# Performance work log

Hardware: AMD Instinct MI355X
Metric: run time of the kernel (lower is better)

## Reference

```python
import jax, jax.numpy as jnp
import numpy as np

B_GRAPHS, N2, FDIM, HEADS = 128, 32, 256, 4
TOTAL = 262144


def setup_inputs() -> dict:
    key = jax.random.key(0)
    ks = jax.random.split(key, 6)
    # sorted graph ids, guaranteed to cover all B_GRAPHS values
    batch = jnp.sort(jnp.concatenate([
        jax.random.randint(ks[0], (TOTAL - B_GRAPHS,), 0, B_GRAPHS),
        jnp.arange(B_GRAPHS)])).astype(jnp.int32)
    x = jax.random.normal(ks[1], (TOTAL, FDIM), jnp.float32)
    queries = jax.random.normal(ks[2], (1, N2, FDIM), jnp.float32)
    s = 1.0 / np.sqrt(FDIM)
    in_proj_w = jax.random.uniform(ks[3], (3 * FDIM, FDIM), jnp.float32, -s, s)
    in_proj_b = jnp.zeros((3 * FDIM,), jnp.float32)
    out_proj_w = jax.random.uniform(ks[4], (FDIM, FDIM), jnp.float32, -s, s)
    out_proj_b = jnp.zeros((FDIM,), jnp.float32)
    return {"x": x, "batch": batch, "queries": queries,
            "in_proj_w": in_proj_w, "in_proj_b": in_proj_b,
            "out_proj_w": out_proj_w, "out_proj_b": out_proj_b}


def reference(x, batch, queries, in_proj_w, in_proj_b, out_proj_w, out_proj_b):
    F = x.shape[-1]
    H = HEADS
    d = F // H
    B = int(batch.max()) + 1
    counts = jnp.bincount(batch, length=B)                      # [B]
    N_max = int(counts.max())
    offsets = jnp.concatenate([jnp.zeros((1,), counts.dtype), jnp.cumsum(counts)[:-1]])
    pos = jnp.arange(batch.shape[0]) - offsets[batch]           # position within segment
    # ragged -> padded scatter (equivalent of the python loop)
    x_padded = jnp.zeros((B, N_max, F), x.dtype).at[batch, pos].set(x)
    valid = jnp.arange(N_max)[None, :] < counts[:, None]        # [B, N_max], True = real token

    Wq, Wk, Wv = in_proj_w[:F], in_proj_w[F:2 * F], in_proj_w[2 * F:]
    bq, bk, bv = in_proj_b[:F], in_proj_b[F:2 * F], in_proj_b[2 * F:]

    scale = 1.0 / np.sqrt(d)
    q = (queries[0] @ Wq.T + bq).reshape(N2, H, d) * scale      # [N2, H, d] (shared over B)
    k = (x_padded @ Wk.T + bk).reshape(B, N_max, H, d)
    v = (x_padded @ Wv.T + bv).reshape(B, N_max, H, d)

    scores = jnp.einsum('qhd,bkhd->bhqk', q, k)                 # [B, H, N2, N_max]
    scores = jnp.where(valid[:, None, None, :], scores, -jnp.inf)
    attn = jax.nn.softmax(scores, axis=-1)
    out = jnp.einsum('bhqk,bkhd->bqhd', attn, v).reshape(B, N2, F)
    out = out @ out_proj_w.T + out_proj_b
    return out.reshape(B * N2, F)
```

## Files before the change

### kernel.cpp

```cpp
#include <hip/hip_runtime.h>
#include <hip/hip_bf16.h>

typedef __bf16 bf16x8 __attribute__((ext_vector_type(8)));
typedef float  f32x4  __attribute__((ext_vector_type(4)));

#define MFMA16(a,b,c) __builtin_amdgcn_mfma_f32_16x16x32_bf16((a),(b),(c),0,0,0)

__device__ __forceinline__ unsigned short f2bf(float f){
  unsigned int u = __float_as_uint(f);
  u += 0x7fffu + ((u >> 16) & 1u);
  return (unsigned short)(u >> 16);
}

__device__ __forceinline__ unsigned int cvtpk(float lo, float hi){
  unsigned int r;
  asm("v_cvt_pk_bf16_f32 %0, %1, %2" : "=v"(r) : "v"(lo), "v"(hi));
  return r;
}

__device__ __forceinline__ void block_sync(){
  asm volatile("s_waitcnt lgkmcnt(0)" ::: "memory");
  __builtin_amdgcn_s_barrier();
}

constexpr float SCALE_LOG2E = 0.125f * 1.4426950408889634f;

__global__ void k_prep(const float* __restrict__ queries, const float* __restrict__ ipw,
                       const float* __restrict__ ipb, const float* __restrict__ opw,
                       const float* __restrict__ opb, const int* __restrict__ batch,
                       int total, int* __restrict__ starts,
                       unsigned short* __restrict__ AqF,
                       unsigned short* __restrict__ Cmat, float* __restrict__ cvec)
{
  __shared__ __align__(16) float sh[256];
  __shared__ __align__(16) float sh2[256];
  const int t = threadIdx.x, bid = blockIdx.x;

  if (bid < 32){
    const int q = bid;
    sh[t] = queries[q*256 + t];
    __syncthreads();
    const float* wr = ipw + (size_t)t*256;
    float acc = 0.f;
    #pragma unroll 8
    for (int j = 0; j < 256; j += 4){
      float4 wv = *reinterpret_cast<const float4*>(wr + j);
      float4 qv = *reinterpret_cast<const float4*>(&sh[j]);
      acc += wv.x*qv.x + wv.y*qv.y + wv.z*qv.z + wv.w*qv.w;
    }
    sh2[t] = acc + ipb[t];
    __syncthreads();
    #pragma unroll
    for (int h = 0; h < 4; h++){
      const float* wk = ipw + (size_t)(256 + h*64)*256 + t;
      float a2 = 0.f;
      #pragma unroll 8
      for (int d = 0; d < 64; d++) a2 += sh2[h*64 + d] * wk[(size_t)d*256];
      const int dst = ((h*2 + (q>>4))*8 + (t>>5))*512 + (((t>>3)&3)*16 + (q&15))*8 + (t&7);
      AqF[dst] = f2bf(a2 * SCALE_LOG2E);
    }
  } else if (bid < 288){
    const int g = bid - 32;
    sh[t] = opw[(size_t)g*256 + t];
    __syncthreads();
    #pragma unroll
    for (int h = 0; h < 4; h++){
      const float* wv = ipw + (size_t)(512 + h*64)*256 + t;
      float acc = 0.f;
      #pragma unroll 8
      for (int d = 0; d < 64; d++) acc += wv[(size_t)d*256] * sh[h*64 + d];
      Cmat[(size_t)g*1024 + h*256 + t] = f2bf(acc);
    }
    sh2[t] = ipb[512 + t] * sh[t];
    __syncthreads();
    for (int off = 128; off > 0; off >>= 1){
      if (t < off) sh2[t] += sh2[t + off];
      __syncthreads();
    }
    if (t == 0) cvec[g] = sh2[0] + opb[g];
  } else {
    const int sb = bid - 288;
    const int i0 = sb*1024 + t*4;
    if (i0 + 3 < total){
      if (i0 == 0) starts[0] = 0;
      const int4 b4 = *reinterpret_cast<const int4*>(batch + i0);
      if (b4.y != b4.x) starts[b4.y] = i0 + 1;
      if (b4.z != b4.y) starts[b4.z] = i0 + 2;
      if (b4.w != b4.z) starts[b4.w] = i0 + 3;
      if (i0 + 4 < total){
        const int nxt = batch[i0 + 4];
        if (nxt != b4.w) starts[nxt] = i0 + 4;
      } else {
        starts[128] = total;
      }
    }
  }
}


#define LOADC(c_) { \
  const int c0_ = (c_)*32; \
  _Pragma("unroll") \
  for (int n = 0; n < 4; n++){ \
    int nl_ = c0_ + nq*4 + n; nl_ = nl_ < cnt-1 ? nl_ : cnt-1; \
    rA[n] = *reinterpret_cast<const float2*>(xg + (size_t)nl_*256 + fp*2); } }

#define STAGE(xsP, xtP) { \
  _Pragma("unroll") \
  for (int n = 0; n < 4; n++) \
    *reinterpret_cast<unsigned int*>(&(xsP)[(nq*4 + n)*264 + fp*2]) = cvtpk(rA[n].x, rA[n].y); \
  { const int f0_ = fp*2; \
    uint2 w0_; w0_.x = cvtpk(rA[0].x, rA[1].x); w0_.y = cvtpk(rA[2].x, rA[3].x); \
    *reinterpret_cast<uint2*>(reinterpret_cast<char*>(xtP) + ((f0_*80 + nq*8) ^ (((f0_>>2)&7)<<4))) = w0_; \
    const int f1_ = fp*2 + 1; \
    uint2 w1_; w1_.x = cvtpk(rA[0].y, rA[1].y); w1_.y = cvtpk(rA[2].y, rA[3].y); \
    *reinterpret_cast<uint2*>(reinterpret_cast<char*>(xtP) + ((f1_*80 + nq*8) ^ (((f1_>>2)&7)<<4))) = w1_; } }

__global__ __launch_bounds__(1024, 4) void k_attn(
    const float* __restrict__ x, const int* __restrict__ starts,
    const unsigned short* __restrict__ AqF,
    float* __restrict__ partO, float* __restrict__ partL)
{
  __shared__ __align__(16) unsigned short xsub[2][32*264];
  __shared__ __align__(16) unsigned short xT  [3][256*40];
  __shared__ __align__(16) unsigned short Plds[2][128*40];
  __shared__ __align__(16) float lred[2][128];

  const int tid = threadIdx.x;
  const int wave = tid >> 6, lane = tid & 63, lg = lane >> 4, li = lane & 15;
  const int rg = wave >> 1, bsel = wave & 1;
  const int fs = wave * 16;
  const int nq = tid >> 7, fp = tid & 127;
  const int bid = blockIdx.x;
  const int g = bid >> 1, s = bid & 1;
  const int s0 = starts[g], s1 = starts[g+1];
  const int cntg = s1 - s0;
  const int half = (cntg + 1) >> 1;
  const int nstart = s0 + s*half;
  int cnt = cntg - s*half; cnt = cnt < 0 ? 0 : (cnt > half ? half : cnt);
  const int chunks = (cnt + 31) >> 5;
  const float* xg = x + (size_t)nstart*256;

  bf16x8 bfragS[8];
  #pragma unroll
  for (int kb = 0; kb < 8; kb++)
    bfragS[kb] = *reinterpret_cast<const bf16x8*>(AqF + (size_t)(rg*8 + kb)*512 + lane*8);

  f32x4 oacc[8];
  #pragma unroll
  for (int i = 0; i < 8; i++) oacc[i] = f32x4{0.f,0.f,0.f,0.f};
  float rsum = 0.f;

  float2 rA[4];
  if (chunks > 0){
    LOADC(0);
    STAGE(xsub[0], xT[0]);
    if (chunks > 1) LOADC(1);
    block_sync();
  }

  int cur3 = 0;
  for (int c = 0; c < chunks; ++c){
    const int cur2 = c & 1;
    const int nxt3 = (cur3 == 2) ? 0 : cur3 + 1;

    f32x4 sacc = f32x4{0.f,0.f,0.f,0.f};
    __builtin_amdgcn_s_setprio(1);
    #pragma unroll
    for (int kb = 0; kb < 8; kb++){
      const bf16x8 af = *reinterpret_cast<const bf16x8*>(&xsub[cur2][(bsel*16 + li)*264 + kb*32 + lg*8]);
      sacc = MFMA16(af, bfragS[kb], sacc);
    }
    __builtin_amdgcn_s_setprio(0);

    const int nodebase = c*32 + bsel*16 + lg*4;
    float p[4];
    #pragma unroll
    for (int r = 0; r < 4; r++){
      p[r] = (nodebase + r < cnt) ? __builtin_exp2f(sacc[r]) : 0.f;
      rsum += p[r];
    }
    {
      const int row = rg*16 + li;
      uint2 w; w.x = cvtpk(p[0], p[1]); w.y = cvtpk(p[2], p[3]);
      *reinterpret_cast<uint2*>(reinterpret_cast<char*>(Plds[cur2])
          + ((row*80 + bsel*32 + lg*8) ^ (((row>>2)&7)<<4))) = w;
    }

    if (c + 1 < chunks){
      STAGE(xsub[cur2 ^ 1], xT[nxt3]);
      if (c + 2 < chunks) LOADC(c + 2);
    }

    block_sync();

    const char* xtC = reinterpret_cast<const char*>(xT[cur3]);
    const int fr = fs + li;
    const bf16x8 bv = *reinterpret_cast<const bf16x8*>(xtC + (((fr*80 + lg*16)) ^ (((fr>>2)&7)<<4)));
    const char* plC = reinterpret_cast<const char*>(Plds[cur2]);
    __builtin_amdgcn_s_setprio(1);
    #pragma unroll
    for (int rt = 0; rt < 8; rt++){
      const int prow = rt*16 + li;
      const bf16x8 pa = *reinterpret_cast<const bf16x8*>(plC + (((prow*80 + lg*16)) ^ (((prow>>2)&7)<<4)));
      oacc[rt] = MFMA16(pa, bv, oacc[rt]);
    }
    __builtin_amdgcn_s_setprio(0);
    cur3 = nxt3;
  }

  rsum += __shfl_xor(rsum, 16);
  rsum += __shfl_xor(rsum, 32);
  if (lane < 16) lred[bsel][rg*16 + li] = rsum;
  block_sync();
  const int pbase = bid*128;
  if (tid < 128) partL[pbase + tid] = lred[0][tid] + lred[1][tid];

  #pragma unroll
  for (int rt = 0; rt < 8; rt++){
    #pragma unroll
    for (int r = 0; r < 4; r++){
      partO[(size_t)(pbase + rt*16 + lg*4 + r)*256 + fs + li] = oacc[rt][r];
    }
  }
}

__global__ __launch_bounds__(512, 1) void k_out(
    const float* __restrict__ partO, const float* __restrict__ partL,
    const unsigned short* __restrict__ Cmat, const float* __restrict__ cvec,
    float* __restrict__ out)
{
  __shared__ __align__(16) unsigned short plds[16*1024];
  __shared__ float sinv[64];
  const int tid = threadIdx.x;
  const int g = blockIdx.x >> 1, qh = blockIdx.x & 1;
  const int p0 = 2*g, p1 = 2*g + 1;
  if (tid < 64){
    const int h = tid >> 4, qr = tid & 15;
    const int row = h*32 + qh*16 + qr;
    const float L = partL[p0*128 + row] + partL[p1*128 + row];
    sinv[tid] = 1.f / L;
  }
  __syncthreads();
  #pragma unroll
  for (int i = 0; i < 8; i++){
    const int idx = tid + i*512;
    const int qr = idx >> 8;
    const int cg = idx & 255;
    const int h = cg >> 6, f4 = (cg & 63)*4;
    const int row = h*32 + qh*16 + qr;
    const float4 o0 = *reinterpret_cast<const float4*>(&partO[(size_t)(p0*128 + row)*256 + f4]);
    const float4 o1 = *reinterpret_cast<const float4*>(&partO[(size_t)(p1*128 + row)*256 + f4]);
    const float sc = sinv[h*16 + qr];
    uint2 w; w.x = cvtpk((o0.x+o1.x)*sc, (o0.y+o1.y)*sc);
             w.y = cvtpk((o0.z+o1.z)*sc, (o0.w+o1.w)*sc);
    const int col4 = cg*4;
    const int bc = (col4*2) ^ ((qr & 7) << 4);
    *reinterpret_cast<uint2*>(reinterpret_cast<char*>(plds) + qr*2048 + bc) = w;
  }
  __syncthreads();
  const int wave = tid >> 6, lane = tid & 63, lg = lane >> 4, li = lane & 15;
  f32x4 acc0 = {0.f,0.f,0.f,0.f}, acc1 = {0.f,0.f,0.f,0.f};
  const float cv0 = cvec[wave*32 + li], cv1 = cvec[wave*32 + 16 + li];
  const unsigned short* cb0 = Cmat + (size_t)(wave*32 + li)*1024;
  const unsigned short* cb1 = Cmat + (size_t)(wave*32 + 16 + li)*1024;
  #pragma unroll 8
  for (int kb = 0; kb < 32; kb++){
    const int bc = ((kb*32 + lg*8)*2) ^ ((li & 7) << 4);
    const bf16x8 aa = *reinterpret_cast<const bf16x8*>(reinterpret_cast<const char*>(plds) + li*2048 + bc);
    const bf16x8 b0 = *reinterpret_cast<const bf16x8*>(cb0 + kb*32 + lg*8);
    const bf16x8 b1 = *reinterpret_cast<const bf16x8*>(cb1 + kb*32 + lg*8);
    acc0 = MFMA16(aa, b0, acc0);
    acc1 = MFMA16(aa, b1, acc1);
  }
  #pragma unroll
  for (int r = 0; r < 4; r++){
    const int q = lg*4 + r;
    const size_t orow = (size_t)(g*32 + qh*16 + q)*256;
    out[orow + wave*32 + li]      = acc0[r] + cv0;
    out[orow + wave*32 + 16 + li] = acc1[r] + cv1;
  }
}


extern "C" void kernel_launch(void* const* d_in, const int* in_sizes, int n_in,
                              void* d_out, int out_size, void* d_ws, size_t ws_size,
                              hipStream_t stream)
{
  const float* x       = (const float*)d_in[0];
  const int*   batch   = (const int*)d_in[1];
  const float* queries = (const float*)d_in[2];
  const float* ipw     = (const float*)d_in[3];
  const float* ipb     = (const float*)d_in[4];
  const float* opw     = (const float*)d_in[5];
  const float* opb     = (const float*)d_in[6];
  float* out = (float*)d_out;
  const int total = in_sizes[1];

  char* w = (char*)d_ws;
  int*            starts = (int*)(w);
  unsigned short* AqF    = (unsigned short*)(w + 36*1024);
  unsigned short* Cmat   = (unsigned short*)(w + 102*1024);
  float*          cvec   = (float*)(w + 616*1024);
  float*          partO  = (float*)(w + (size_t)1024*1024);
  float*          partL  = (float*)(w + (size_t)1024*1024 + (size_t)256*128*256*4);

  k_prep<<<544, 256, 0, stream>>>(queries, ipw, ipb, opw, opb, batch, total,
                                  starts, AqF, Cmat, cvec);
  k_attn<<<256, 1024, 0, stream>>>(x, starts, AqF, partO, partL);
  k_out<<<256, 512, 0, stream>>>(partO, partL, Cmat, cvec, out);
}
```

Baseline: 114.4 us.

## Specialize waves into score/softmax producers and PV-accumulation consumers

The 16 waves of the attention kernel are split into two roles. Waves 0-7 compute the QK scores, the exp and the row sums for two query fragments each, and write P into LDS. Waves 8-15 run the P·V MFMAs for 32 feature columns each. With one barrier per chunk on each side, score computation for chunk c+1 can overlap the PV accumulation of chunk c, instead of every wave serializing both phases around the barrier. The cost is that each wave keeps twice as many fragments and accumulators in registers, and the two roles may be unevenly loaded because the producer waves also do the exp and conversion work.

```diff
diff --git a/kernel.cpp b/kernel.cpp
--- a/kernel.cpp
+++ b/kernel.cpp
@@ -128,8 +128,6 @@
 
   const int tid = threadIdx.x;
   const int wave = tid >> 6, lane = tid & 63, lg = lane >> 4, li = lane & 15;
-  const int rg = wave >> 1, bsel = wave & 1;
-  const int fs = wave * 16;
   const int nq = tid >> 7, fp = tid & 127;
   const int bid = blockIdx.x;
   const int g = bid >> 1, s = bid & 1;
@@ -140,16 +138,7 @@
   int cnt = cntg - s*half; cnt = cnt < 0 ? 0 : (cnt > half ? half : cnt);
   const int chunks = (cnt + 31) >> 5;
   const float* xg = x + (size_t)nstart*256;
-
-  bf16x8 bfragS[8];
-  #pragma unroll
-  for (int kb = 0; kb < 8; kb++)
-    bfragS[kb] = *reinterpret_cast<const bf16x8*>(AqF + (size_t)(rg*8 + kb)*512 + lane*8);
-
-  f32x4 oacc[8];
-  #pragma unroll
-  for (int i = 0; i < 8; i++) oacc[i] = f32x4{0.f,0.f,0.f,0.f};
-  float rsum = 0.f;
+  const int pbase = bid*128;
 
   float2 rA[4];
   if (chunks > 0){
@@ -159,70 +148,115 @@
     block_sync();
   }
 
-  int cur3 = 0;
-  for (int c = 0; c < chunks; ++c){
-    const int cur2 = c & 1;
-    const int nxt3 = (cur3 == 2) ? 0 : cur3 + 1;
-
-    f32x4 sacc = f32x4{0.f,0.f,0.f,0.f};
-    __builtin_amdgcn_s_setprio(1);
-    #pragma unroll
-    for (int kb = 0; kb < 8; kb++){
-      const bf16x8 af = *reinterpret_cast<const bf16x8*>(&xsub[cur2][(bsel*16 + li)*264 + kb*32 + lg*8]);
-      sacc = MFMA16(af, bfragS[kb], sacc);
-    }
-    __builtin_amdgcn_s_setprio(0);
-
-    const int nodebase = c*32 + bsel*16 + lg*4;
-    float p[4];
-    #pragma unroll
-    for (int r = 0; r < 4; r++){
-      p[r] = (nodebase + r < cnt) ? __builtin_exp2f(sacc[r]) : 0.f;
-      rsum += p[r];
-    }
-    {
-      const int row = rg*16 + li;
-      uint2 w; w.x = cvtpk(p[0], p[1]); w.y = cvtpk(p[2], p[3]);
-      *reinterpret_cast<uint2*>(reinterpret_cast<char*>(Plds[cur2])
-          + ((row*80 + bsel*32 + lg*8) ^ (((row>>2)&7)<<4))) = w;
-    }
-
-    if (c + 1 < chunks){
-      STAGE(xsub[cur2 ^ 1], xT[nxt3]);
-      if (c + 2 < chunks) LOADC(c + 2);
-    }
-
-    block_sync();
-
-    const char* xtC = reinterpret_cast<const char*>(xT[cur3]);
-    const int fr = fs + li;
-    const bf16x8 bv = *reinterpret_cast<const bf16x8*>(xtC + (((fr*80 + lg*16)) ^ (((fr>>2)&7)<<4)));
-    const char* plC = reinterpret_cast<const char*>(Plds[cur2]);
-    __builtin_amdgcn_s_setprio(1);
+  if (wave < 8){
+    const int rg2 = wave >> 1, bsel = wave & 1;
+    bf16x8 bfragS[2][8];
+    #pragma unroll
+    for (int rf = 0; rf < 2; rf++)
+      #pragma unroll
+      for (int kb = 0; kb < 8; kb++)
+        bfragS[rf][kb] = *reinterpret_cast<const bf16x8*>(AqF + (size_t)((rg2*2 + rf)*8 + kb)*512 + lane*8);
+
+    float rsum0 = 0.f, rsum1 = 0.f;
+    const int row0 = rg2*32 + li, row1 = rg2*32 + 16 + li;
+    const int pbyte0 = (row0*80 + bsel*32 + lg*8) ^ (((row0>>2)&7)<<4);
+    const int pbyte1 = (row1*80 + bsel*32 + lg*8) ^ (((row1>>2)&7)<<4);
+
+    int cur3 = 0;
+    for (int c = 0; c < chunks; ++c){
+      const int cur2 = c & 1;
+      const int nxt3 = (cur3 == 2) ? 0 : cur3 + 1;
+
+      f32x4 sc0 = f32x4{0.f,0.f,0.f,0.f}, sc1 = f32x4{0.f,0.f,0.f,0.f};
+      __builtin_amdgcn_s_setprio(1);
+      #pragma unroll
+      for (int kb = 0; kb < 8; kb++){
+        const bf16x8 af = *reinterpret_cast<const bf16x8*>(&xsub[cur2][(bsel*16 + li)*264 + kb*32 + lg*8]);
+        sc0 = MFMA16(af, bfragS[0][kb], sc0);
+        sc1 = MFMA16(af, bfragS[1][kb], sc1);
+      }
+      __builtin_amdgcn_s_setprio(0);
+
+      const int nodebase = c*32 + bsel*16 + lg*4;
+      float p0[4], p1[4];
+      #pragma unroll
+      for (int r = 0; r < 4; r++){
+        const bool v = (nodebase + r) < cnt;
+        p0[r] = v ? __builtin_exp2f(sc0[r]) : 0.f;
+        p1[r] = v ? __builtin_exp2f(sc1[r]) : 0.f;
+        rsum0 += p0[r]; rsum1 += p1[r];
+      }
+      {
+        char* pl = reinterpret_cast<char*>(Plds[cur2]);
+        uint2 w0; w0.x = cvtpk(p0[0], p0[1]); w0.y = cvtpk(p0[2], p0[3]);
+        uint2 w1; w1.x = cvtpk(p1[0], p1[1]); w1.y = cvtpk(p1[2], p1[3]);
+        *reinterpret_cast<uint2*>(pl + pbyte0) = w0;
+        *reinterpret_cast<uint2*>(pl + pbyte1) = w1;
+      }
+
+      if (c + 1 < chunks){
+        STAGE(xsub[cur2 ^ 1], xT[nxt3]);
+        if (c + 2 < chunks) LOADC(c + 2);
+      }
+      block_sync();
+      cur3 = nxt3;
+    }
+
+    rsum0 += __shfl_xor(rsum0, 16); rsum0 += __shfl_xor(rsum0, 32);
+    rsum1 += __shfl_xor(rsum1, 16); rsum1 += __shfl_xor(rsum1, 32);
+    if (lane < 16){
+      lred[bsel][rg2*32 + li]      = rsum0;
+      lred[bsel][rg2*32 + 16 + li] = rsum1;
+    }
+  } else {
+    const int pw = wave - 8, fs = pw*32;
+    f32x4 oacc[8][2];
+    #pragma unroll
+    for (int i = 0; i < 8; i++){ oacc[i][0] = f32x4{0.f,0.f,0.f,0.f}; oacc[i][1] = f32x4{0.f,0.f,0.f,0.f}; }
+    const int fr0 = fs + li, fr1 = fs + 16 + li;
+    const int bvb0 = (fr0*80 + lg*16) ^ (((fr0>>2)&7)<<4);
+    const int bvb1 = (fr1*80 + lg*16) ^ (((fr1>>2)&7)<<4);
+
+    int cur3 = 0;
+    for (int c = 0; c < chunks; ++c){
+      const int cur2 = c & 1;
+      const int nxt3 = (cur3 == 2) ? 0 : cur3 + 1;
+
+      if (c + 1 < chunks){
+        STAGE(xsub[cur2 ^ 1], xT[nxt3]);
+        if (c + 2 < chunks) LOADC(c + 2);
+      }
+      block_sync();
+
+      const char* xtC = reinterpret_cast<const char*>(xT[cur3]);
+      const bf16x8 bv0 = *reinterpret_cast<const bf16x8*>(xtC + bvb0);
+      const bf16x8 bv1 = *reinterpret_cast<const bf16x8*>(xtC + bvb1);
+      const char* plC = reinterpret_cast<const char*>(Plds[cur2]);
+      __builtin_amdgcn_s_setprio(1);
+      #pragma unroll
+      for (int rt = 0; rt < 8; rt++){
+        const int prow = rt*16 + li;
+        const bf16x8 pa = *reinterpret_cast<const bf16x8*>(plC + ((prow*80 + lg*16) ^ (((prow>>2)&7)<<4)));
+        oacc[rt][0] = MFMA16(pa, bv0, oacc[rt][0]);
+        oacc[rt][1] = MFMA16(pa, bv1, oacc[rt][1]);
+      }
+      __builtin_amdgcn_s_setprio(0);
+      cur3 = nxt3;
+    }
+
     #pragma unroll
     for (int rt = 0; rt < 8; rt++){
-      const int prow = rt*16 + li;
-      const bf16x8 pa = *reinterpret_cast<const bf16x8*>(plC + (((prow*80 + lg*16)) ^ (((prow>>2)&7)<<4)));
-      oacc[rt] = MFMA16(pa, bv, oacc[rt]);
-    }
-    __builtin_amdgcn_s_setprio(0);
-    cur3 = nxt3;
-  }
-
-  rsum += __shfl_xor(rsum, 16);
-  rsum += __shfl_xor(rsum, 32);
-  if (lane < 16) lred[bsel][rg*16 + li] = rsum;
+      #pragma unroll
+      for (int r = 0; r < 4; r++){
+        const size_t orow = (size_t)(pbase + rt*16 + lg*4 + r)*256;
+        partO[orow + fs + li]      = oacc[rt][0][r];
+        partO[orow + fs + 16 + li] = oacc[rt][1][r];
+      }
+    }
+  }
+
   block_sync();
-  const int pbase = bid*128;
   if (tid < 128) partL[pbase + tid] = lred[0][tid] + lred[1][tid];
-
-  #pragma unroll
-  for (int rt = 0; rt < 8; rt++){
-    #pragma unroll
-    for (int r = 0; r < 4; r++){
-      partO[(size_t)(pbase + rt*16 + lg*4 + r)*256 + fs + li] = oacc[rt][r];
-    }
-  }
 }
 
 __global__ __launch_bounds__(512, 1) void k_out(
```

Result: faster. 105.0 us (-8.2%).
